# Kernel optimization log

Hardware: AMD Instinct MI355X
Metric: run time of the kernel (lower is better)

## Reference

```python
import jax, jax.numpy as jnp
import numpy as np


def setup_inputs() -> dict:
    key = jax.random.key(0)
    ks = jax.random.split(key, 8)
    B, N, D, S = 4, 16384, 512, 512
    x = jax.random.normal(ks[0], (B, N, D), dtype=jnp.float32)
    jx = jnp.sort(jax.random.randint(ks[1], (N,), 0, S, dtype=jnp.int64))
    scale = 1.0 / np.sqrt(D)
    Wf = jax.random.normal(ks[2], (D, D), dtype=jnp.float32) * scale
    bf = jax.random.normal(ks[3], (D,), dtype=jnp.float32) * scale
    Wg = jax.random.normal(ks[4], (D, D), dtype=jnp.float32) * scale
    bg = jax.random.normal(ks[5], (D,), dtype=jnp.float32) * scale
    Wh = jax.random.normal(ks[6], (D, D), dtype=jnp.float32) * scale
    bh = jax.random.normal(ks[7], (D,), dtype=jnp.float32) * scale
    return {"x": x, "jx": jx, "num_segments": S, "Wf": Wf, "bf": bf,
            "Wg": Wg, "bg": bg, "Wh": Wh, "bh": bh}


def reference(x, jx, num_segments, Wf, bf, Wg, bg, Wh, bh):
    # x: [B, N, D]; jx: [N] segment ids; segments along axis 1.
    fx = jnp.einsum('bnd,ed->bne', x, Wf) + bf  # f(x)
    gx = jnp.einsum('bnd,ed->bne', x, Wg) + bg  # g(x)
    # move N to leading axis so jax.ops.segment_* apply: [N, B, D]
    gx_t = jnp.transpose(gx, (1, 0, 2))
    fx_t = jnp.transpose(fx, (1, 0, 2))
    # scatter_softmax over segments (numerically stable)
    m = jax.ops.segment_max(gx_t, jx, num_segments=num_segments)  # [S, B, D]
    e = jnp.exp(gx_t - m[jx])
    denom = jax.ops.segment_sum(e, jx, num_segments=num_segments)  # [S, B, D]
    w = e / denom[jx]  # [N, B, D]
    # weighted scatter-sum
    y_t = jax.ops.segment_sum(fx_t * w, jx, num_segments=num_segments)  # [S, B, D]
    y = jnp.transpose(y_t, (1, 0, 2))  # [B, S, D]
    hy = jnp.einsum('bsd,ed->bse', y, Wh) + bh
    # expand=True: gather back to per-element
    return hy[:, jx]  # [B, N, D]
```

## Files before the change

### kernel.cpp

```cpp
#include <hip/hip_runtime.h>
#include <stdint.h>

#define B_ 4
#define N_ 16384
#define D_ 512
#define S_ 512

typedef __attribute__((ext_vector_type(8))) short bf16x8;
typedef __attribute__((ext_vector_type(4))) float f32x4;

__device__ __forceinline__ float bf2f(unsigned short u) {
  union { unsigned int i; float f; } v; v.i = ((unsigned int)u) << 16; return v.f;
}
__device__ __forceinline__ unsigned short f2bf(float f) {
  unsigned int x = __float_as_uint(f);
  return (unsigned short)((x + 0x7FFFu + ((x >> 16) & 1u)) >> 16);
}
__device__ __forceinline__ float ldf(const void* p, long i, bool f32) {
  return f32 ? ((const float*)p)[i] : bf2f(((const unsigned short*)p)[i]);
}

__device__ __forceinline__ bool jx_is_i64(const int* jx32) { return jx32[N_ - 1] == 0; }
__device__ __forceinline__ int seg_id(const int* jx32, int n, bool i64) {
  return i64 ? jx32[2 * n] : jx32[n];
}

__global__ void detect_f32(const unsigned short* __restrict__ x, int* __restrict__ flag) {
  __shared__ int cnt[256];
  int c = 0;
#pragma unroll
  for (int i = 0; i < 8; i++) {
    unsigned short w = x[threadIdx.x * 8 + i];
    int e = (w >> 7) & 0xFF;
    if (e == 0 || (e >= 100 && e <= 140)) c++;
  }
  cnt[threadIdx.x] = c;
  __syncthreads();
  for (int s = 128; s > 0; s >>= 1) {
    if ((int)threadIdx.x < s) cnt[threadIdx.x] += cnt[threadIdx.x + s];
    __syncthreads();
  }
  if (threadIdx.x == 0) *flag = (cnt[0] < (2048 * 9) / 10) ? 1 : 0;
}

__global__ void seg_bounds(const int* __restrict__ jx, int* __restrict__ st) {
  int s = blockIdx.x * blockDim.x + threadIdx.x;
  if (s > S_) return;
  bool i64 = jx_is_i64(jx);
  int lo = 0, hi = N_;
  while (lo < hi) {
    int mid = (lo + hi) >> 1;
    if (seg_id(jx, mid, i64) < s) lo = mid + 1; else hi = mid;
  }
  st[s] = lo;
}

__global__ void prep(const void* __restrict__ Wf, const void* __restrict__ bfv,
                     const void* __restrict__ Wg, const void* __restrict__ bgv,
                     const void* __restrict__ Wh, const void* __restrict__ bhv,
                     const int* __restrict__ flag,
                     unsigned short* __restrict__ Wfg, unsigned short* __restrict__ biasfg,
                     unsigned short* __restrict__ Whb, unsigned short* __restrict__ bhb) {
  const bool f32 = *flag != 0;
  int idx = blockIdx.x * 256 + threadIdx.x;
  if (idx < 524288) {
    int e = idx >> 9, d = idx & 511;
    float v = (e < 512) ? ldf(Wf, (long)e * 512 + d, f32)
                        : ldf(Wg, (long)(e - 512) * 512 + d, f32);
    Wfg[idx] = f2bf(v);
  } else if (idx < 786432) {
    int j = idx - 524288;
    Whb[j] = f2bf(ldf(Wh, j, f32));
  } else if (idx < 787456) {
    int j = idx - 786432;
    biasfg[j] = f2bf(j < 512 ? ldf(bfv, j, f32) : ldf(bgv, j - 512, f32));
  } else if (idx < 787968) {
    int j = idx - 787456;
    bhb[j] = f2bf(ldf(bhv, j, f32));
  }
}

#define BK 32

__global__ __launch_bounds__(256, 2)
void gemm_bias_bt(const void* __restrict__ A, const unsigned short* __restrict__ Bm,
                  const unsigned short* __restrict__ bias,
                  unsigned short* __restrict__ Cf, unsigned short* __restrict__ Cg,
                  int E, int Kdim, int splitcol, const int* __restrict__ aflag) {
  __shared__ __align__(16) unsigned short As[128 * BK];
  __shared__ __align__(16) unsigned short Bs[128 * BK];
  const bool af32 = aflag ? (*aflag != 0) : false;
  const int tid  = threadIdx.x;
  const int w    = tid >> 6;
  const int lane = tid & 63;
  const int wm   = w >> 1, wn = w & 1;
  const int m0   = blockIdx.y * 128;
  const int n0   = blockIdx.x * 128;
  const int l15  = lane & 15, l4 = lane >> 4;
  const int srow = tid >> 1;
  const int sk0  = (tid & 1) * 16;

  f32x4 acc[4][4];
#pragma unroll
  for (int i = 0; i < 4; i++)
#pragma unroll
    for (int j = 0; j < 4; j++) acc[i][j] = (f32x4){0.f, 0.f, 0.f, 0.f};

  for (int kt = 0; kt < Kdim; kt += BK) {
    __syncthreads();
    {
      const size_t gbase = (size_t)(m0 + srow) * Kdim + kt + sk0;
      bf16x8 v0, v1;
      if (af32) {
        const float4* ap = (const float4*)((const float*)A + gbase);
        float4 a0 = ap[0], a1 = ap[1], a2 = ap[2], a3 = ap[3];
        v0[0]=f2bf(a0.x); v0[1]=f2bf(a0.y); v0[2]=f2bf(a0.z); v0[3]=f2bf(a0.w);
        v0[4]=f2bf(a1.x); v0[5]=f2bf(a1.y); v0[6]=f2bf(a1.z); v0[7]=f2bf(a1.w);
        v1[0]=f2bf(a2.x); v1[1]=f2bf(a2.y); v1[2]=f2bf(a2.z); v1[3]=f2bf(a2.w);
        v1[4]=f2bf(a3.x); v1[5]=f2bf(a3.y); v1[6]=f2bf(a3.z); v1[7]=f2bf(a3.w);
      } else {
        const unsigned short* ap = (const unsigned short*)A + gbase;
        v0 = *(const bf16x8*)ap;
        v1 = *(const bf16x8*)(ap + 8);
      }
      *(bf16x8*)&As[srow * BK + sk0]     = v0;
      *(bf16x8*)&As[srow * BK + sk0 + 8] = v1;
    }
    {
      const unsigned short* bp = Bm + (size_t)(n0 + srow) * Kdim + kt + sk0;
      *(bf16x8*)&Bs[srow * BK + sk0]     = *(const bf16x8*)bp;
      *(bf16x8*)&Bs[srow * BK + sk0 + 8] = *(const bf16x8*)(bp + 8);
    }
    __syncthreads();

    bf16x8 a[4], b[4];
#pragma unroll
    for (int i = 0; i < 4; i++)
      a[i] = *(const bf16x8*)&As[(wm * 64 + i * 16 + l15) * BK + l4 * 8];
#pragma unroll
    for (int j = 0; j < 4; j++)
      b[j] = *(const bf16x8*)&Bs[(wn * 64 + j * 16 + l15) * BK + l4 * 8];
#pragma unroll
    for (int i = 0; i < 4; i++)
#pragma unroll
      for (int j = 0; j < 4; j++)
        acc[i][j] = __builtin_amdgcn_mfma_f32_16x16x32_bf16(a[i], b[j], acc[i][j], 0, 0, 0);
  }

#pragma unroll
  for (int j = 0; j < 4; j++) {
    const int col = n0 + wn * 64 + j * 16 + l15;
    const float bv = bf2f(bias[col]);
    unsigned short* base; int cc, stride;
    if (col < splitcol) { base = Cf; cc = col; stride = splitcol; }
    else { base = Cg; cc = col - splitcol; stride = E - splitcol; }
#pragma unroll
    for (int i = 0; i < 4; i++) {
      const int rowb = m0 + wm * 64 + i * 16 + l4 * 4;
#pragma unroll
      for (int r = 0; r < 4; r++)
        base[(size_t)(rowb + r) * stride + cc] = f2bf(acc[i][j][r] + bv);
    }
  }
}

__global__ __launch_bounds__(256)
void seg_softmax(const unsigned short* __restrict__ f, const unsigned short* __restrict__ g,
                 const int* __restrict__ segst, unsigned short* __restrict__ y) {
  const int s = blockIdx.x, b = blockIdx.y;
  const int st = segst[s], en = segst[s + 1];
  const int d0 = threadIdx.x * 2;
  float den0 = 0.f, den1 = 0.f, y0 = 0.f, y1 = 0.f;
  for (int n = st; n < en; n++) {
    const size_t off = (size_t)(b * N_ + n) * 512 + d0;
    const unsigned int fp = *(const unsigned int*)(f + off);
    const unsigned int gp = *(const unsigned int*)(g + off);
    const float f0 = bf2f((unsigned short)fp), f1 = bf2f((unsigned short)(fp >> 16));
    const float g0 = bf2f((unsigned short)gp), g1 = bf2f((unsigned short)(gp >> 16));
    const float e0 = __expf(g0), e1 = __expf(g1);
    den0 += e0; den1 += e1;
    y0 += f0 * e0; y1 += f1 * e1;
  }
  const float r0 = (en > st) ? y0 / den0 : 0.f;
  const float r1 = (en > st) ? y1 / den1 : 0.f;
  unsigned short* yr = y + (size_t)(b * S_ + s) * 512 + d0;
  yr[0] = f2bf(r0);
  yr[1] = f2bf(r1);
}

__global__ __launch_bounds__(256)
void gather_out(const unsigned short* __restrict__ hy, const int* __restrict__ jx,
                void* __restrict__ out, const int* __restrict__ flag) {
  const bool f32 = *flag != 0;
  const int gid  = blockIdx.x * 256 + threadIdx.x;
  const int wid  = gid >> 6;
  const int lane = gid & 63;
  const int b = wid >> 14;
  const int n = wid & (N_ - 1);
  const bool i64 = jx_is_i64(jx);
  const int s = seg_id(jx, n, i64);
  const bf16x8 v = *(const bf16x8*)(hy + (size_t)(b * S_ + s) * 512 + lane * 8);
  if (f32) {
    float* dst = (float*)out + (size_t)wid * 512 + lane * 8;
#pragma unroll
    for (int t = 0; t < 8; t++) dst[t] = bf2f((unsigned short)v[t]);
  } else {
    *(bf16x8*)((unsigned short*)out + (size_t)wid * 512 + lane * 8) = v;
  }
}

extern "C" void kernel_launch(void* const* d_in, const int* in_sizes, int n_in,
                              void* d_out, int out_size, void* d_ws, size_t ws_size,
                              hipStream_t stream) {
  const void* x  = d_in[0];
  const int* jx  = (const int*)d_in[1];
  const void* Wf = d_in[3];
  const void* bf = d_in[4];
  const void* Wg = d_in[5];
  const void* bg = d_in[6];
  const void* Wh = d_in[7];
  const void* bh = d_in[8];

  char* ws = (char*)d_ws;
  int* flag              = (int*)(ws + 0);
  int* segst             = (int*)(ws + 4096);
  unsigned short* biasfg = (unsigned short*)(ws + 8192);
  unsigned short* bhb    = (unsigned short*)(ws + 16384);
  unsigned short* Wfg    = (unsigned short*)(ws + 32768);
  unsigned short* Whb    = (unsigned short*)(ws + 1081344);
  unsigned short* y_ws   = (unsigned short*)(ws + 1605632);
  unsigned short* hy_ws  = (unsigned short*)(ws + 3702784);
  unsigned short* gbuf   = (unsigned short*)(ws + 5799936);
  unsigned short* fbuf   = (unsigned short*)d_out;

  detect_f32<<<1, 256, 0, stream>>>((const unsigned short*)x, flag);
  seg_bounds<<<3, 256, 0, stream>>>(jx, segst);
  prep<<<3078, 256, 0, stream>>>(Wf, bf, Wg, bg, Wh, bh, flag, Wfg, biasfg, Whb, bhb);
  gemm_bias_bt<<<dim3(8, 512), 256, 0, stream>>>(x, Wfg, biasfg, fbuf, gbuf,
                                                 1024, 512, 512, flag);
  seg_softmax<<<dim3(S_, B_), 256, 0, stream>>>(fbuf, gbuf, segst, y_ws);
  gemm_bias_bt<<<dim3(4, 16), 256, 0, stream>>>(y_ws, Whb, bhb, hy_ws, hy_ws,
                                                512, 512, 512, nullptr);
  gather_out<<<16384, 256, 0, stream>>>(hy_ws, jx, d_out, flag);
}
```

Before: 450.8 us.

## Pre-convert x to bf16 and stage GEMM tiles with global_load_lds

Adds a separate cvt_x pass that converts x to bf16, so the GEMM no longer converts fp32 inside its load loop. GEMM tiles are now staged with direct global-to-LDS loads (global_load_lds). A 1D grid remaps tiles so each XCD works on a contiguous band of rows, improving L2 locality. The gbuf intermediate moves into the second half of the output buffer. The trade-off is an extra full read and write of x through the conversion kernel.

```diff
diff --git a/kernel.cpp b/kernel.cpp
--- a/kernel.cpp
+++ b/kernel.cpp
@@ -18,6 +18,12 @@
 }
 __device__ __forceinline__ float ldf(const void* p, long i, bool f32) {
   return f32 ? ((const float*)p)[i] : bf2f(((const unsigned short*)p)[i]);
+}
+__device__ __forceinline__ void gl_lds16(void* lds_base, const void* g) {
+  __builtin_amdgcn_global_load_lds(
+      (const __attribute__((address_space(1))) unsigned int*)g,
+      (__attribute__((address_space(3))) unsigned int*)lds_base,
+      16, 0, 0);
 }
 
 __device__ __forceinline__ bool jx_is_i64(const int* jx32) { return jx32[N_ - 1] == 0; }
@@ -69,36 +75,55 @@
                         : ldf(Wg, (long)(e - 512) * 512 + d, f32);
     Wfg[idx] = f2bf(v);
   } else if (idx < 786432) {
-    int j = idx - 524288;
-    Whb[j] = f2bf(ldf(Wh, j, f32));
+    Whb[idx - 524288] = f2bf(ldf(Wh, idx - 524288, f32));
   } else if (idx < 787456) {
     int j = idx - 786432;
     biasfg[j] = f2bf(j < 512 ? ldf(bfv, j, f32) : ldf(bgv, j - 512, f32));
   } else if (idx < 787968) {
-    int j = idx - 787456;
-    bhb[j] = f2bf(ldf(bhv, j, f32));
-  }
+    bhb[idx - 787456] = f2bf(ldf(bhv, idx - 787456, f32));
+  }
+}
+
+__global__ __launch_bounds__(256)
+void cvt_x(const void* __restrict__ x, const int* __restrict__ flag,
+           unsigned short* __restrict__ xb) {
+  const bool f32 = *flag != 0;
+  const size_t i0 = ((size_t)blockIdx.x * 256 + threadIdx.x) * 8;
+  bf16x8 v;
+  if (f32) {
+    const float4* p = (const float4*)((const float*)x + i0);
+    float4 a = p[0], b = p[1];
+    v[0]=f2bf(a.x); v[1]=f2bf(a.y); v[2]=f2bf(a.z); v[3]=f2bf(a.w);
+    v[4]=f2bf(b.x); v[5]=f2bf(b.y); v[6]=f2bf(b.z); v[7]=f2bf(b.w);
+  } else {
+    v = *(const bf16x8*)((const unsigned short*)x + i0);
+  }
+  *(bf16x8*)(xb + i0) = v;
 }
 
 #define BK 32
 
 __global__ __launch_bounds__(256, 2)
-void gemm_bias_bt(const void* __restrict__ A, const unsigned short* __restrict__ Bm,
-                  const unsigned short* __restrict__ bias,
-                  unsigned short* __restrict__ Cf, unsigned short* __restrict__ Cg,
-                  int E, int Kdim, int splitcol, const int* __restrict__ aflag) {
+void gemm_bt(const unsigned short* __restrict__ A, const unsigned short* __restrict__ Bm,
+             const unsigned short* __restrict__ bias,
+             unsigned short* __restrict__ Cf, unsigned short* __restrict__ Cg,
+             int E, int Kdim, int splitcol, int tilesM, int tilesN) {
   __shared__ __align__(16) unsigned short As[128 * BK];
   __shared__ __align__(16) unsigned short Bs[128 * BK];
-  const bool af32 = aflag ? (*aflag != 0) : false;
+  const int L = blockIdx.x;
+  const int xcd = L & 7, local = L >> 3;
+  const int rowsPerX = tilesM >> 3;
+  const int tm = xcd * rowsPerX + local / tilesN;
+  const int tn = local % tilesN;
+  const int m0 = tm * 128, n0 = tn * 128;
+
   const int tid  = threadIdx.x;
   const int w    = tid >> 6;
   const int lane = tid & 63;
   const int wm   = w >> 1, wn = w & 1;
-  const int m0   = blockIdx.y * 128;
-  const int n0   = blockIdx.x * 128;
   const int l15  = lane & 15, l4 = lane >> 4;
-  const int srow = tid >> 1;
-  const int sk0  = (tid & 1) * 16;
+  const int srow = lane >> 2;
+  const int scol = (lane & 3) * 8;
 
   f32x4 acc[4][4];
 #pragma unroll
@@ -108,28 +133,11 @@
 
   for (int kt = 0; kt < Kdim; kt += BK) {
     __syncthreads();
-    {
-      const size_t gbase = (size_t)(m0 + srow) * Kdim + kt + sk0;
-      bf16x8 v0, v1;
-      if (af32) {
-        const float4* ap = (const float4*)((const float*)A + gbase);
-        float4 a0 = ap[0], a1 = ap[1], a2 = ap[2], a3 = ap[3];
-        v0[0]=f2bf(a0.x); v0[1]=f2bf(a0.y); v0[2]=f2bf(a0.z); v0[3]=f2bf(a0.w);
-        v0[4]=f2bf(a1.x); v0[5]=f2bf(a1.y); v0[6]=f2bf(a1.z); v0[7]=f2bf(a1.w);
-        v1[0]=f2bf(a2.x); v1[1]=f2bf(a2.y); v1[2]=f2bf(a2.z); v1[3]=f2bf(a2.w);
-        v1[4]=f2bf(a3.x); v1[5]=f2bf(a3.y); v1[6]=f2bf(a3.z); v1[7]=f2bf(a3.w);
-      } else {
-        const unsigned short* ap = (const unsigned short*)A + gbase;
-        v0 = *(const bf16x8*)ap;
-        v1 = *(const bf16x8*)(ap + 8);
-      }
-      *(bf16x8*)&As[srow * BK + sk0]     = v0;
-      *(bf16x8*)&As[srow * BK + sk0 + 8] = v1;
-    }
-    {
-      const unsigned short* bp = Bm + (size_t)(n0 + srow) * Kdim + kt + sk0;
-      *(bf16x8*)&Bs[srow * BK + sk0]     = *(const bf16x8*)bp;
-      *(bf16x8*)&Bs[srow * BK + sk0 + 8] = *(const bf16x8*)(bp + 8);
+#pragma unroll
+    for (int r = 0; r < 2; r++) {
+      const int rb = (r * 4 + w) * 16;
+      gl_lds16(&As[rb * BK], A + (size_t)(m0 + rb + srow) * Kdim + kt + scol);
+      gl_lds16(&Bs[rb * BK], Bm + (size_t)(n0 + rb + srow) * Kdim + kt + scol);
     }
     __syncthreads();
 
@@ -230,16 +238,18 @@
   unsigned short* Whb    = (unsigned short*)(ws + 1081344);
   unsigned short* y_ws   = (unsigned short*)(ws + 1605632);
   unsigned short* hy_ws  = (unsigned short*)(ws + 3702784);
-  unsigned short* gbuf   = (unsigned short*)(ws + 5799936);
+  unsigned short* xb     = (unsigned short*)(ws + 8388608);
   unsigned short* fbuf   = (unsigned short*)d_out;
+  unsigned short* gbuf   = (unsigned short*)d_out + (size_t)B_ * N_ * D_;
 
   detect_f32<<<1, 256, 0, stream>>>((const unsigned short*)x, flag);
   seg_bounds<<<3, 256, 0, stream>>>(jx, segst);
   prep<<<3078, 256, 0, stream>>>(Wf, bf, Wg, bg, Wh, bh, flag, Wfg, biasfg, Whb, bhb);
-  gemm_bias_bt<<<dim3(8, 512), 256, 0, stream>>>(x, Wfg, biasfg, fbuf, gbuf,
-                                                 1024, 512, 512, flag);
+  cvt_x<<<16384, 256, 0, stream>>>(x, flag, xb);
+  gemm_bt<<<4096, 256, 0, stream>>>(xb, Wfg, biasfg, fbuf, gbuf,
+                                    1024, 512, 512, 512, 8);
   seg_softmax<<<dim3(S_, B_), 256, 0, stream>>>(fbuf, gbuf, segst, y_ws);
-  gemm_bias_bt<<<dim3(4, 16), 256, 0, stream>>>(y_ws, Whb, bhb, hy_ws, hy_ws,
-                                                512, 512, 512, nullptr);
+  gemm_bt<<<64, 256, 0, stream>>>(y_ws, Whb, bhb, hy_ws, hy_ws,
+                                  512, 512, 512, 16, 4);
   gather_out<<<16384, 256, 0, stream>>>(hy_ws, jx, d_out, flag);
 }
```

Measured after the change: 399.1 us. 11.5% less time.
